# Kernel tuning notes

Hardware: AMD Instinct MI355X
Metric: run time of the kernel (lower is better)

The kernel has to match this reference:

```python
import jax, jax.numpy as jnp
import numpy as np


def setup_inputs() -> dict:
    key = jax.random.key(0)
    k1, k2 = jax.random.split(key)
    p1 = jax.random.normal(k1, (4, 8192, 3), dtype=jnp.float32)
    p2 = jax.random.normal(k2, (4, 8192, 3), dtype=jnp.float32)
    return {"p1": p1, "p2": p2}


def reference(p1, p2):
    # dist[b, n, m] = ||p1[b, n] - p2[b, m]||^2  (faithful to broadcasted diff)
    diff = p1[:, :, None, :] - p2[:, None, :, :]          # [B, N, M, 3]
    dist = jnp.sum(diff * diff, axis=-1)                  # [B, N, M]
    p1_to_p2 = jnp.min(dist, axis=-1)                     # [B, N]
    p2_to_p1 = jnp.min(dist, axis=-2)                     # [B, M]
    chamfer = (p1_to_p2.mean(axis=-1) + p2_to_p1.mean(axis=-1)).mean()
    return chamfer
```

## Files before the change

### kernel.cpp

```cpp
#include <hip/hip_runtime.h>

#define THREADS 256
#define QPT 8
#define Q2  (QPT / 2)
#define SLICES 32
#define NPTS 8192
#define BATCH 4
#define SLICE (NPTS / SLICES)

typedef float f2 __attribute__((ext_vector_type(2)));


__global__ void chamfer_init(unsigned int* mins, float* out) {
    int i = blockIdx.x * blockDim.x + threadIdx.x;
    mins[i] = 0x7F800000u;
    if (i == 0) out[0] = 0.0f;
}

__global__ __launch_bounds__(THREADS) void chamfer_main(
    const float* __restrict__ p1, const float* __restrict__ p2,
    unsigned int* __restrict__ mins)
{
    const int tid  = threadIdx.x;
    const int bz   = blockIdx.z;
    const int dir  = bz >> 2;
    const int b    = bz & 3;
    const int qbase = blockIdx.x * (THREADS * QPT);
    const int tbase = blockIdx.y * SLICE;

    const float* __restrict__ qsrc = (dir == 0) ? p1 : p2;
    const float* __restrict__ tsrc = (dir == 0) ? p2 : p1;

    __shared__ float4 tgt[SLICE];
    {
        const float* tp = tsrc + ((size_t)b * NPTS + tbase) * 3;
        for (int k = tid; k < SLICE; k += THREADS) {
            float x = tp[k * 3 + 0];
            float y = tp[k * 3 + 1];
            float z = tp[k * 3 + 2];
            tgt[k] = make_float4(-2.0f * x, -2.0f * y, -2.0f * z,
                                 fmaf(x, x, fmaf(y, y, z * z)));
        }
    }

    f2 ax2[Q2], ay2[Q2], az2[Q2], a2q[Q2], best2[Q2];
#pragma unroll
    for (int j = 0; j < Q2; ++j) {
        const int qa = qbase + (2 * j + 0) * THREADS + tid;
        const int qb = qbase + (2 * j + 1) * THREADS + tid;
        const float* pa = qsrc + ((size_t)b * NPTS + qa) * 3;
        const float* pb = qsrc + ((size_t)b * NPTS + qb) * 3;
        ax2[j] = f2{pa[0], pb[0]};
        ay2[j] = f2{pa[1], pb[1]};
        az2[j] = f2{pa[2], pb[2]};
        a2q[j].x = fmaf(ax2[j].x, ax2[j].x, fmaf(ay2[j].x, ay2[j].x, az2[j].x * az2[j].x));
        a2q[j].y = fmaf(ax2[j].y, ax2[j].y, fmaf(ay2[j].y, ay2[j].y, az2[j].y * az2[j].y));
        best2[j] = f2{3.0e38f, 3.0e38f};
    }

    __syncthreads();

#pragma unroll 4
    for (int m = 0; m < SLICE; m += 2) {
        float4 ta = tgt[m];
        float4 tb = tgt[m + 1];
        f2 tax = {ta.x, ta.x}, tay = {ta.y, ta.y}, taz = {ta.z, ta.z}, taw = {ta.w, ta.w};
        f2 tbx = {tb.x, tb.x}, tby = {tb.y, tb.y}, tbz = {tb.z, tb.z}, tbw = {tb.w, tb.w};
#pragma unroll
        for (int j = 0; j < Q2; ++j) {
            f2 da = __builtin_elementwise_fma(ax2[j], tax,
                     __builtin_elementwise_fma(ay2[j], tay,
                      __builtin_elementwise_fma(az2[j], taz, taw)));
            f2 db = __builtin_elementwise_fma(ax2[j], tbx,
                     __builtin_elementwise_fma(ay2[j], tby,
                      __builtin_elementwise_fma(az2[j], tbz, tbw)));
            best2[j].x = fminf(fminf(best2[j].x, da.x), db.x);
            best2[j].y = fminf(fminf(best2[j].y, da.y), db.y);
        }
    }

    unsigned int* mbase = mins + ((size_t)dir * BATCH + b) * NPTS;
#pragma unroll
    for (int j = 0; j < Q2; ++j) {
        float va = fmaxf(best2[j].x + a2q[j].x, 0.0f);
        float vb = fmaxf(best2[j].y + a2q[j].y, 0.0f);
        atomicMin(&mbase[qbase + (2 * j + 0) * THREADS + tid], __float_as_uint(va));
        atomicMin(&mbase[qbase + (2 * j + 1) * THREADS + tid], __float_as_uint(vb));
    }
}

__global__ __launch_bounds__(THREADS) void chamfer_reduce(
    const uint4* __restrict__ mins, float* __restrict__ out)
{
    const int i = blockIdx.x * THREADS + threadIdx.x;
    uint4 u = mins[i];
    float s = __uint_as_float(u.x) + __uint_as_float(u.y)
            + __uint_as_float(u.z) + __uint_as_float(u.w);
#pragma unroll
    for (int off = 32; off >= 1; off >>= 1)
        s += __shfl_down(s, off, 64);
    __shared__ float partial[THREADS / 64];
    if ((threadIdx.x & 63) == 0) partial[threadIdx.x >> 6] = s;
    __syncthreads();
    if (threadIdx.x == 0) {
        float tot = 0.0f;
#pragma unroll
        for (int w = 0; w < THREADS / 64; ++w) tot += partial[w];
        atomicAdd(out, tot * (1.0f / (BATCH * NPTS)));
    }
}

extern "C" void kernel_launch(void* const* d_in, const int* in_sizes, int n_in,
                              void* d_out, int out_size, void* d_ws, size_t ws_size,
                              hipStream_t stream) {
    const float* p1 = (const float*)d_in[0];
    const float* p2 = (const float*)d_in[1];
    unsigned int* mins = (unsigned int*)d_ws;
    float* out = (float*)d_out;

    chamfer_init<<<(2 * BATCH * NPTS) / THREADS, THREADS, 0, stream>>>(mins, out);

    dim3 grid(NPTS / (THREADS * QPT), SLICES, 2 * BATCH);
    chamfer_main<<<grid, THREADS, 0, stream>>>(p1, p2, mins);

    chamfer_reduce<<<(2 * BATCH * NPTS) / (4 * THREADS), THREADS, 0, stream>>>(
        (const uint4*)mins, out);
}
```

Baseline: 96.08 us.

## Stream targets from global memory with packed FMA asm and fuse final reduction

```diff
diff --git a/kernel.cpp b/kernel.cpp
--- a/kernel.cpp
+++ b/kernel.cpp
@@ -1,25 +1,33 @@
 #include <hip/hip_runtime.h>
 
 #define THREADS 256
-#define QPT 8
+#define QPT 4
 #define Q2  (QPT / 2)
 #define SLICES 32
 #define NPTS 8192
 #define BATCH 4
 #define SLICE (NPTS / SLICES)
+#define TG 4
+#define NGRP (SLICE / TG)
+#define NMINS (2 * BATCH * NPTS)
+#define NBLOCKS ((NPTS / (THREADS * QPT)) * SLICES * 2 * BATCH)
 
 typedef float f2 __attribute__((ext_vector_type(2)));
 
 
-__global__ void chamfer_init(unsigned int* mins, float* out) {
+__global__ void chamfer_init(unsigned int* mins, unsigned int* counter, float* out) {
     int i = blockIdx.x * blockDim.x + threadIdx.x;
     mins[i] = 0x7F800000u;
-    if (i == 0) out[0] = 0.0f;
+    if (i == 0) {
+        if (counter) *counter = 0u;
+        else out[0] = 0.0f;
+    }
 }
 
-__global__ __launch_bounds__(THREADS) void chamfer_main(
+__global__ __launch_bounds__(THREADS, 4) void chamfer_main(
     const float* __restrict__ p1, const float* __restrict__ p2,
-    unsigned int* __restrict__ mins)
+    unsigned int* __restrict__ mins, unsigned int* __restrict__ counter,
+    float* __restrict__ out)
 {
     const int tid  = threadIdx.x;
     const int bz   = blockIdx.z;
@@ -31,61 +39,103 @@
     const float* __restrict__ qsrc = (dir == 0) ? p1 : p2;
     const float* __restrict__ tsrc = (dir == 0) ? p2 : p1;
 
-    __shared__ float4 tgt[SLICE];
-    {
-        const float* tp = tsrc + ((size_t)b * NPTS + tbase) * 3;
-        for (int k = tid; k < SLICE; k += THREADS) {
-            float x = tp[k * 3 + 0];
-            float y = tp[k * 3 + 1];
-            float z = tp[k * 3 + 2];
-            tgt[k] = make_float4(-2.0f * x, -2.0f * y, -2.0f * z,
-                                 fmaf(x, x, fmaf(y, y, z * z)));
-        }
-    }
-
-    f2 ax2[Q2], ay2[Q2], az2[Q2], a2q[Q2], best2[Q2];
+    f2 sx[Q2], sy[Q2], sz[Q2], best[Q2];
 #pragma unroll
     for (int j = 0; j < Q2; ++j) {
         const int qa = qbase + (2 * j + 0) * THREADS + tid;
         const int qb = qbase + (2 * j + 1) * THREADS + tid;
         const float* pa = qsrc + ((size_t)b * NPTS + qa) * 3;
         const float* pb = qsrc + ((size_t)b * NPTS + qb) * 3;
-        ax2[j] = f2{pa[0], pb[0]};
-        ay2[j] = f2{pa[1], pb[1]};
-        az2[j] = f2{pa[2], pb[2]};
-        a2q[j].x = fmaf(ax2[j].x, ax2[j].x, fmaf(ay2[j].x, ay2[j].x, az2[j].x * az2[j].x));
-        a2q[j].y = fmaf(ax2[j].y, ax2[j].y, fmaf(ay2[j].y, ay2[j].y, az2[j].y * az2[j].y));
-        best2[j] = f2{3.0e38f, 3.0e38f};
+        sx[j] = f2{-2.0f * pa[0], -2.0f * pb[0]};
+        sy[j] = f2{-2.0f * pa[1], -2.0f * pb[1]};
+        sz[j] = f2{-2.0f * pa[2], -2.0f * pb[2]};
+        best[j] = f2{3.0e38f, 3.0e38f};
     }
 
-    __syncthreads();
+    int zoff;
+    asm("v_mov_b32 %0, 0" : "=v"(zoff));
+    const float* tbp = tsrc + ((size_t)b * NPTS + tbase) * 3 + zoff;
 
-#pragma unroll 4
-    for (int m = 0; m < SLICE; m += 2) {
-        float4 ta = tgt[m];
-        float4 tb = tgt[m + 1];
-        f2 tax = {ta.x, ta.x}, tay = {ta.y, ta.y}, taz = {ta.z, ta.z}, taw = {ta.w, ta.w};
-        f2 tbx = {tb.x, tb.x}, tby = {tb.y, tb.y}, tbz = {tb.z, tb.z}, tbw = {tb.w, tb.w};
+#pragma unroll 2
+    for (int g = 0; g < NGRP; ++g) {
+        const f2* gp = (const f2*)(tbp + 12 * g);
+        f2 P0 = gp[0], P1 = gp[1], P2 = gp[2], P3 = gp[3], P4 = gp[4], P5 = gp[5];
+        float w0 = fmaf(P0.x, P0.x, fmaf(P0.y, P0.y, P1.x * P1.x));
+        float w1 = fmaf(P1.y, P1.y, fmaf(P2.x, P2.x, P2.y * P2.y));
+        float w2 = fmaf(P3.x, P3.x, fmaf(P3.y, P3.y, P4.x * P4.x));
+        float w3 = fmaf(P4.y, P4.y, fmaf(P5.x, P5.x, P5.y * P5.y));
+        f2 wp01 = {w0, w1}, wp23 = {w2, w3};
 #pragma unroll
         for (int j = 0; j < Q2; ++j) {
-            f2 da = __builtin_elementwise_fma(ax2[j], tax,
-                     __builtin_elementwise_fma(ay2[j], tay,
-                      __builtin_elementwise_fma(az2[j], taz, taw)));
-            f2 db = __builtin_elementwise_fma(ax2[j], tbx,
-                     __builtin_elementwise_fma(ay2[j], tby,
-                      __builtin_elementwise_fma(az2[j], tbz, tbw)));
-            best2[j].x = fminf(fminf(best2[j].x, da.x), db.x);
-            best2[j].y = fminf(fminf(best2[j].y, da.y), db.y);
+            f2 d0, d1, d2, d3;
+            asm("v_pk_fma_f32 %0, %1, %2, %3 op_sel:[0,0,0] op_sel_hi:[1,0,0]"
+                : "=v"(d0) : "v"(sz[j]), "v"(P1), "v"(wp01));
+            asm("v_pk_fma_f32 %0, %1, %2, %0 op_sel:[0,1,0] op_sel_hi:[1,1,1]"
+                : "+v"(d0) : "v"(sy[j]), "v"(P0));
+            asm("v_pk_fma_f32 %0, %1, %2, %0 op_sel:[0,0,0] op_sel_hi:[1,0,1]"
+                : "+v"(d0) : "v"(sx[j]), "v"(P0));
+            asm("v_pk_fma_f32 %0, %1, %2, %3 op_sel:[0,1,1] op_sel_hi:[1,1,1]"
+                : "=v"(d1) : "v"(sz[j]), "v"(P2), "v"(wp01));
+            asm("v_pk_fma_f32 %0, %1, %2, %0 op_sel:[0,0,0] op_sel_hi:[1,0,1]"
+                : "+v"(d1) : "v"(sy[j]), "v"(P2));
+            asm("v_pk_fma_f32 %0, %1, %2, %0 op_sel:[0,1,0] op_sel_hi:[1,1,1]"
+                : "+v"(d1) : "v"(sx[j]), "v"(P1));
+            asm("v_pk_fma_f32 %0, %1, %2, %3 op_sel:[0,0,0] op_sel_hi:[1,0,0]"
+                : "=v"(d2) : "v"(sz[j]), "v"(P4), "v"(wp23));
+            asm("v_pk_fma_f32 %0, %1, %2, %0 op_sel:[0,1,0] op_sel_hi:[1,1,1]"
+                : "+v"(d2) : "v"(sy[j]), "v"(P3));
+            asm("v_pk_fma_f32 %0, %1, %2, %0 op_sel:[0,0,0] op_sel_hi:[1,0,1]"
+                : "+v"(d2) : "v"(sx[j]), "v"(P3));
+            asm("v_pk_fma_f32 %0, %1, %2, %3 op_sel:[0,1,1] op_sel_hi:[1,1,1]"
+                : "=v"(d3) : "v"(sz[j]), "v"(P5), "v"(wp23));
+            asm("v_pk_fma_f32 %0, %1, %2, %0 op_sel:[0,0,0] op_sel_hi:[1,0,1]"
+                : "+v"(d3) : "v"(sy[j]), "v"(P5));
+            asm("v_pk_fma_f32 %0, %1, %2, %0 op_sel:[0,1,0] op_sel_hi:[1,1,1]"
+                : "+v"(d3) : "v"(sx[j]), "v"(P4));
+            best[j].x = fminf(fminf(best[j].x, d0.x), d1.x);
+            best[j].x = fminf(fminf(best[j].x, d2.x), d3.x);
+            best[j].y = fminf(fminf(best[j].y, d0.y), d1.y);
+            best[j].y = fminf(fminf(best[j].y, d2.y), d3.y);
         }
     }
 
     unsigned int* mbase = mins + ((size_t)dir * BATCH + b) * NPTS;
 #pragma unroll
     for (int j = 0; j < Q2; ++j) {
-        float va = fmaxf(best2[j].x + a2q[j].x, 0.0f);
-        float vb = fmaxf(best2[j].y + a2q[j].y, 0.0f);
+        float qa2 = 0.25f * fmaf(sx[j].x, sx[j].x, fmaf(sy[j].x, sy[j].x, sz[j].x * sz[j].x));
+        float qb2 = 0.25f * fmaf(sx[j].y, sx[j].y, fmaf(sy[j].y, sy[j].y, sz[j].y * sz[j].y));
+        float va = fmaxf(best[j].x + qa2, 0.0f);
+        float vb = fmaxf(best[j].y + qb2, 0.0f);
         atomicMin(&mbase[qbase + (2 * j + 0) * THREADS + tid], __float_as_uint(va));
         atomicMin(&mbase[qbase + (2 * j + 1) * THREADS + tid], __float_as_uint(vb));
+    }
+
+    if (counter) {
+        __threadfence();
+        __syncthreads();
+        __shared__ unsigned int tick;
+        if (tid == 0)
+            tick = __hip_atomic_fetch_add(counter, 1u, __ATOMIC_ACQ_REL,
+                                          __HIP_MEMORY_SCOPE_AGENT);
+        __syncthreads();
+        if (tick == NBLOCKS - 1) {
+            float s = 0.0f;
+            for (int i = tid; i < NMINS; i += THREADS) {
+                unsigned int u = __hip_atomic_load(&mins[i], __ATOMIC_RELAXED,
+                                                   __HIP_MEMORY_SCOPE_AGENT);
+                s += __uint_as_float(u);
+            }
+#pragma unroll
+            for (int off = 32; off >= 1; off >>= 1)
+                s += __shfl_down(s, off, 64);
+            __shared__ float part[THREADS / 64];
+            if ((tid & 63) == 0) part[tid >> 6] = s;
+            __syncthreads();
+            if (tid == 0) {
+                float tot = part[0] + part[1] + part[2] + part[3];
+                out[0] = tot * (1.0f / (BATCH * NPTS));
+            }
+        }
     }
 }
 
@@ -117,12 +167,15 @@
     const float* p2 = (const float*)d_in[1];
     unsigned int* mins = (unsigned int*)d_ws;
     float* out = (float*)d_out;
+    const bool fused = ws_size >= (size_t)(NMINS + 1) * sizeof(unsigned int);
+    unsigned int* counter = fused ? (mins + NMINS) : nullptr;
 
-    chamfer_init<<<(2 * BATCH * NPTS) / THREADS, THREADS, 0, stream>>>(mins, out);
+    chamfer_init<<<NMINS / THREADS, THREADS, 0, stream>>>(mins, counter, out);
 
     dim3 grid(NPTS / (THREADS * QPT), SLICES, 2 * BATCH);
-    chamfer_main<<<grid, THREADS, 0, stream>>>(p1, p2, mins);
+    chamfer_main<<<grid, THREADS, 0, stream>>>(p1, p2, mins, counter, out);
 
-    chamfer_reduce<<<(2 * BATCH * NPTS) / (4 * THREADS), THREADS, 0, stream>>>(
-        (const uint4*)mins, out);
+    if (!fused)
+        chamfer_reduce<<<NMINS / (4 * THREADS), THREADS, 0, stream>>>(
+            (const uint4*)mins, out);
 }
```

Measured after the change: 300.6 us. 3.13x slower.
